# Performance work log

Measured on AMD Instinct MI355X. Metric: run time of the kernel, lower is better.

The kernel has to match this reference:

```python
import jax, jax.numpy as jnp
import numpy as np

N, H, W, SD = 64, 22, 22, 8
HW = H * W


def _conv(x, w, b):
    # 3x3 SAME conv, NCHW / OIHW
    y = jax.lax.conv_general_dilated(x, w, (1, 1), 'SAME',
                                     dimension_numbers=('NCHW', 'OIHW', 'NCHW'))
    return y + b[None, :, None, None]


def _bn(x, g, b, eps=1e-5):
    # BatchNorm2d in training mode: batch statistics over (N, H, W)
    m = jnp.mean(x, axis=(0, 2, 3), keepdims=True)
    v = jnp.var(x, axis=(0, 2, 3), keepdims=True)
    return (x - m) * jax.lax.rsqrt(v + eps) * g[None, :, None, None] + b[None, :, None, None]


def setup_inputs() -> dict:
    key = jax.random.key(0)
    ks = iter(jax.random.split(key, 64))
    def kw(shape):  # kaiming-normal fan_in init
        fan_in = int(np.prod(shape[1:]))
        return jax.random.normal(next(ks), shape, jnp.float32) * np.float32(np.sqrt(2.0 / fan_in))
    d = {
        'cost_volume': jax.random.normal(next(ks), (N, HW, H, W), jnp.float32),
        'state_prev': jax.random.normal(next(ks), (N, SD, H, W), jnp.float32),
        'dimp_score_cur': jax.random.normal(next(ks), (N, 1, H, W), jnp.float32),
    }
    for p in ('cv1', 'cv2'):  # two cost-volume processing stacks: conv(1->8)+BN+ReLU, conv(8->1)+BN
        d[p + '_w1'] = kw((8, 1, 3, 3)); d[p + '_b1'] = jnp.zeros(8, jnp.float32)
        d[p + '_g1'] = jnp.ones(8, jnp.float32); d[p + '_be1'] = jnp.zeros(8, jnp.float32)
        d[p + '_w2'] = kw((1, 8, 3, 3)); d[p + '_b2'] = jnp.zeros(1, jnp.float32)
        d[p + '_g2'] = jnp.ones(1, jnp.float32); d[p + '_be2'] = jnp.zeros(1, jnp.float32)
    d['rp1_w'] = kw((64, SD + 2, 3, 3)); d['rp1_b'] = jnp.zeros(64, jnp.float32)
    d['rp2_w'] = kw((32, 64, 3, 3)); d['rp2_b'] = jnp.zeros(32, jnp.float32)
    d['resp_w'] = kw((1, 32, 3, 3)); d['resp_b'] = jnp.zeros(1, jnp.float32)
    for g_ in ('gru_r', 'gru_u', 'gru_o'):  # ConvGRUCell(input=4, hidden=SD, ksz=3)
        d[g_ + 'w'] = kw((SD, 4 + SD, 3, 3)); d[g_ + 'b'] = jnp.zeros(SD, jnp.float32)
    return d


def _fwd(cost_volume, state_prev, dimp_score_cur,
         cv1_w1, cv1_b1, cv1_g1, cv1_be1, cv1_w2, cv1_b2, cv1_g2, cv1_be2,
         cv2_w1, cv2_b1, cv2_g1, cv2_be1, cv2_w2, cv2_b2, cv2_g2, cv2_be2,
         rp1_w, rp1_b, rp2_w, rp2_b, resp_w, resp_b,
         gru_rw, gru_rb, gru_uw, gru_ub, gru_ow, gru_ob):
    n = cost_volume.shape[0]
    # ---- cost volume processing 1: per-map spatial softmax ----
    x = cost_volume.reshape(-1, 1, H, W)                       # (N*HW, 1, H, W)
    p = jax.nn.relu(_bn(_conv(x, cv1_w1, cv1_b1), cv1_g1, cv1_be1))
    p = _bn(_conv(p, cv1_w2, cv1_b2), cv1_g2, cv1_be2)
    p = jax.nn.softmax(p.reshape(-1, HW), axis=1).reshape(-1, 1, H, W)
    # ---- cost volume processing 2: softmax over source positions ----
    p = jax.nn.relu(_bn(_conv(p, cv2_w1, cv2_b1), cv2_g1, cv2_be1))
    p = _bn(_conv(p, cv2_w2, cv2_b2), cv2_g2, cv2_be2)
    p = jax.nn.softmax(p.reshape(n, HW, H, W), axis=1)         # propagation weights (n, p, h, w)
    # ---- confidence ('max') ----
    conf = jnp.max(p, axis=1, keepdims=True)                   # (N, 1, H, W)
    # ---- state propagation: contract over source positions (no (N,HW,C,H,W) intermediate) ----
    s = state_prev.transpose(0, 2, 3, 1).reshape(n, HW, SD)    # (n, p, d)
    prop_h = jnp.einsum('nphw,npd->ndhw', p, s)                # (N, SD, H, W)
    # ---- response prediction ----
    pin = jnp.concatenate([prop_h, dimp_score_cur, conf], axis=1)   # (N, SD+2, H, W)
    r = jax.nn.relu(_conv(pin, rp1_w, rp1_b))
    r = jax.nn.relu(_conv(r, rp2_w, rp2_b))
    fused = jax.nn.sigmoid(_conv(r, resp_w, resp_b))           # (N, 1, H, W)
    # ---- ConvGRU state update ----
    scores_cat = jnp.concatenate([dimp_score_cur, fused], axis=1)   # (N, 2, H, W)
    pool = jnp.max(scores_cat, axis=(2, 3), keepdims=True)          # adaptive max pool to 1x1
    gin = jnp.concatenate([scores_cat, jnp.broadcast_to(pool, scores_cat.shape)], axis=1)  # (N,4,H,W)
    stacked = jnp.concatenate([gin, prop_h], axis=1)           # (N, 4+SD, H, W)
    upd = jax.nn.sigmoid(_conv(stacked, gru_uw, gru_ub))
    rst = jax.nn.sigmoid(_conv(stacked, gru_rw, gru_rb))
    out = jnp.tanh(_conv(jnp.concatenate([gin, prop_h * rst], axis=1), gru_ow, gru_ob))
    state_new = prop_h * (1.0 - upd) + out * upd               # (N, SD, H, W)
    return jnp.concatenate([fused, state_new], axis=1)         # (N, 1+SD, H, W)


def reference(cost_volume, state_prev, dimp_score_cur,
              cv1_w1, cv1_b1, cv1_g1, cv1_be1, cv1_w2, cv1_b2, cv1_g2, cv1_be2,
              cv2_w1, cv2_b1, cv2_g1, cv2_be1, cv2_w2, cv2_b2, cv2_g2, cv2_be2,
              rp1_w, rp1_b, rp2_w, rp2_b, resp_w, resp_b,
              gru_rw, gru_rb, gru_uw, gru_ub, gru_ow, gru_ob):
    return _fwd(cost_volume, state_prev, dimp_score_cur,
                cv1_w1, cv1_b1, cv1_g1, cv1_be1, cv1_w2, cv1_b2, cv1_g2, cv1_be2,
                cv2_w1, cv2_b1, cv2_g1, cv2_be1, cv2_w2, cv2_b2, cv2_g2, cv2_be2,
                rp1_w, rp1_b, rp2_w, rp2_b, resp_w, resp_b,
                gru_rw, gru_rb, gru_uw, gru_ub, gru_ow, gru_ob)
```

## Files before the change

kernel.cpp:

```cpp
#include <hip/hip_runtime.h>

#define HH 22
#define WW 22
#define HWN 484
#define NBATCH 64
#define SDIM 8
#define NMAPS (NBATCH*HWN)
#define PW 24
#define CELLS 576
#define PADW 24
#define PADSZ (PADW*PADW)
#define INVC (1.f/14992384.f)

#define LD9(A, idx) \
  float x0=(A)[(idx)-PW-1], x1=(A)[(idx)-PW], x2=(A)[(idx)-PW+1], \
        x3=(A)[(idx)-1],    x4=(A)[(idx)],    x5=(A)[(idx)+1], \
        x6=(A)[(idx)+PW-1], x7=(A)[(idx)+PW], x8=(A)[(idx)+PW+1]
#define DOT9W(w9, init) \
  fmaf((w9)[0],x0,fmaf((w9)[1],x1,fmaf((w9)[2],x2,fmaf((w9)[3],x3,fmaf((w9)[4],x4, \
  fmaf((w9)[5],x5,fmaf((w9)[6],x6,fmaf((w9)[7],x7,fmaf((w9)[8],x8,(init))))))))))

#define LOAD_NB(arr, bb) do { \
    nb[0]=(arr)[(bb)-PADW-1]; nb[1]=(arr)[(bb)-PADW]; nb[2]=(arr)[(bb)-PADW+1]; \
    nb[3]=(arr)[(bb)-1];      nb[4]=(arr)[(bb)];      nb[5]=(arr)[(bb)+1]; \
    nb[6]=(arr)[(bb)+PADW-1]; nb[7]=(arr)[(bb)+PADW]; nb[8]=(arr)[(bb)+PADW+1]; } while(0)

__global__ __launch_bounds__(576) void k_stats(const float* __restrict__ src,
    const float* __restrict__ w, const float* __restrict__ b,
    float* __restrict__ Sg, float* __restrict__ Qg)
{
    __shared__ float xin[2][CELLS];
    __shared__ float red[16];
    int tid=threadIdx.x;
    int i=tid/PW, j=tid-i*PW;
    bool inter = (i>=1 && i<=22 && j>=1 && j<=22);
    int p=(i-1)*22+(j-1);
    xin[0][tid]=0.f; xin[1][tid]=0.f;
    float accS[8], accQ[8];
#pragma unroll
    for(int c=0;c<8;++c){ accS[c]=0.f; accQ[c]=0.f; }
    int m0=blockIdx.x*16;
    if(inter) xin[0][tid]=src[(size_t)m0*HWN+p];
    __syncthreads();
    for(int mi=0;mi<16;++mi){
        int cur=mi&1;
        float nx=0.f;
        if(mi<15 && inter) nx=src[(size_t)(m0+mi+1)*HWN+p];
        if(inter){
            LD9(xin[cur], tid);
#pragma unroll
            for(int c=0;c<8;++c){
                float y=DOT9W(w+c*9, b[c]);
                accS[c]+=y; accQ[c]=fmaf(y,y,accQ[c]);
            }
        }
        if(mi<15 && inter) xin[cur^1][tid]=nx;
        __syncthreads();
    }
    if(tid<16) red[tid]=0.f;
    __syncthreads();
#pragma unroll
    for(int c=0;c<8;++c){
        float s=accS[c], q=accQ[c];
        for(int o=32;o;o>>=1){ s+=__shfl_down(s,o); q+=__shfl_down(q,o); }
        if((tid&63)==0){ atomicAdd(&red[c],s); atomicAdd(&red[8+c],q); }
    }
    __syncthreads();
    if(tid<8){ atomicAdd(&Sg[tid],red[tid]); atomicAdd(&Qg[tid],red[8+tid]); }
}

__global__ __launch_bounds__(576) void k_convpair(const float* __restrict__ src, float* __restrict__ Ydst,
    const float* __restrict__ w1, const float* __restrict__ b1,
    const float* __restrict__ Sin, const float* __restrict__ Qin,
    const float* __restrict__ g, const float* __restrict__ be,
    const float* __restrict__ w2, const float* __restrict__ b2,
    float* __restrict__ Sg, float* __restrict__ Qg)
{
    __shared__ float xin[2][CELLS];
    __shared__ float z[8][CELLS];
    __shared__ float scs[8], shs[8];
    __shared__ float red[2];
    int tid=threadIdx.x;
    int i=tid/PW, j=tid-i*PW;
    bool inter = (i>=1 && i<=22 && j>=1 && j<=22);
    int p=(i-1)*22+(j-1);
    xin[0][tid]=0.f; xin[1][tid]=0.f;
#pragma unroll
    for(int c=0;c<8;++c) z[c][tid]=0.f;
    if(tid<8){
        float mean=Sin[tid]*INVC;
        float var=fmaf(-mean,mean,Qin[tid]*INVC);
        float sc=g[tid]*rsqrtf(var+1e-5f);
        scs[tid]=sc; shs[tid]=fmaf(-mean,sc,be[tid]);
    }
    float aS=0.f, aQ=0.f;
    float b2v=b2[0];
    int m0=blockIdx.x*16;
    if(inter) xin[0][tid]=src[(size_t)m0*HWN+p];
    __syncthreads();
    for(int mi=0;mi<16;++mi){
        int cur=mi&1;
        float nx=0.f;
        if(mi<15 && inter) nx=src[(size_t)(m0+mi+1)*HWN+p];
        if(inter){
            LD9(xin[cur], tid);
#pragma unroll
            for(int c=0;c<8;++c){
                float y=DOT9W(w1+c*9, b1[c]);
                y=fmaf(y,scs[c],shs[c]);
                z[c][tid]=y>0.f?y:0.f;
            }
        }
        if(mi<15 && inter) xin[cur^1][tid]=nx;
        __syncthreads();
        if(inter){
            float y=b2v;
#pragma unroll
            for(int c=0;c<8;++c){
                LD9(z[c], tid);
                y=DOT9W(w2+c*9, y);
            }
            Ydst[(size_t)(m0+mi)*HWN+p]=y;
            aS+=y; aQ=fmaf(y,y,aQ);
        }
        __syncthreads();
    }
    if(tid<2) red[tid]=0.f;
    __syncthreads();
    for(int o=32;o;o>>=1){ aS+=__shfl_down(aS,o); aQ+=__shfl_down(aQ,o); }
    if((tid&63)==0){ atomicAdd(&red[0],aS); atomicAdd(&red[1],aQ); }
    __syncthreads();
    if(tid==0){ atomicAdd(Sg,red[0]); atomicAdd(Qg,red[1]); }
}

__global__ __launch_bounds__(576) void k_smax_stats(float* __restrict__ Y,
    const float* __restrict__ S2, const float* __restrict__ Q2,
    const float* __restrict__ g2, const float* __restrict__ be2,
    const float* __restrict__ w, const float* __restrict__ b,
    float* __restrict__ Sg, float* __restrict__ Qg)
{
    __shared__ float xin[CELLS];
    __shared__ float red9[9];
    __shared__ float red[16];
    int tid=threadIdx.x;
    int i=tid/PW, j=tid-i*PW;
    bool inter = (i>=1 && i<=22 && j>=1 && j<=22);
    int p=(i-1)*22+(j-1);
    float mean=S2[0]*INVC;
    float var=fmaf(-mean,mean,Q2[0]*INVC);
    float a=g2[0]*rsqrtf(var+1e-5f);
    float sh=fmaf(-mean,a,be2[0]);
    xin[tid]=0.f;
    float accS[8], accQ[8];
#pragma unroll
    for(int c=0;c<8;++c){ accS[c]=0.f; accQ[c]=0.f; }
    int m0=blockIdx.x*16;
    for(int mi=0;mi<16;++mi){
        size_t off=(size_t)(m0+mi)*HWN+p;
        float e = inter ? __expf(fmaf(Y[off],a,sh)) : 0.f;
        float part=e;
        for(int o=32;o;o>>=1) part+=__shfl_down(part,o);
        if((tid&63)==0) red9[tid>>6]=part;
        xin[tid]=e;
        __syncthreads();
        float sum=red9[0]+red9[1]+red9[2]+red9[3]+red9[4]+red9[5]+red9[6]+red9[7]+red9[8];
        float inv=1.f/sum;
        if(inter){
            Y[off]=e*inv;
            LD9(xin, tid);
#pragma unroll
            for(int c=0;c<8;++c){
                float d=DOT9W(w+c*9, 0.f);
                float y=fmaf(inv,d,b[c]);
                accS[c]+=y; accQ[c]=fmaf(y,y,accQ[c]);
            }
        }
        __syncthreads();
    }
    if(tid<16) red[tid]=0.f;
    __syncthreads();
#pragma unroll
    for(int c=0;c<8;++c){
        float s=accS[c], q=accQ[c];
        for(int o=32;o;o>>=1){ s+=__shfl_down(s,o); q+=__shfl_down(q,o); }
        if((tid&63)==0){ atomicAdd(&red[c],s); atomicAdd(&red[8+c],q); }
    }
    __syncthreads();
    if(tid<8){ atomicAdd(&Sg[tid],red[tid]); atomicAdd(&Qg[tid],red[8+tid]); }
}

__global__ __launch_bounds__(512) void k_prop(const float* __restrict__ Y,
    const float* __restrict__ S4, const float* __restrict__ Q4,
    const float* __restrict__ g4, const float* __restrict__ be4,
    const float* __restrict__ state, float* __restrict__ prop, float* __restrict__ conf)
{
    int n=blockIdx.x;
    __shared__ float sst[8*HWN];
    __shared__ float part[4][121][10];
    int tid=threadIdx.x;
    for(int q=tid;q<8*HWN;q+=512) sst[q]=state[(size_t)n*8*HWN + q];
    __syncthreads();
    int tq=tid&127, pc=tid>>7;
    int t=blockIdx.y*121+tq;
    float mean=S4[0]*INVC;
    float var=fmaf(-mean,mean,Q4[0]*INVC);
    float a=g4[0]*rsqrtf(var+1e-5f);
    float sh=fmaf(-mean,a,be4[0]);
    if(tq<121){
        const float* col = Y + (size_t)n*HWN*HWN + t + (size_t)pc*121*HWN;
        const float* sp = sst + pc*121;
        float mx=-1e30f, ssum=0.f;
        float acc[8];
#pragma unroll
        for(int d=0;d<8;++d) acc[d]=0.f;
#pragma unroll 4
        for(int p=0;p<121;++p){
            float v=fmaf(col[(size_t)p*HWN], a, sh);
            float e=__expf(v);
            mx=fmaxf(mx,v); ssum+=e;
#pragma unroll
            for(int d=0;d<8;++d) acc[d]=fmaf(e, sp[d*HWN+p], acc[d]);
        }
        part[pc][tq][0]=ssum; part[pc][tq][1]=mx;
#pragma unroll
        for(int d=0;d<8;++d) part[pc][tq][2+d]=acc[d];
    }
    __syncthreads();
    if(pc==0 && tq<121){
        float ssum=part[0][tq][0]+part[1][tq][0]+part[2][tq][0]+part[3][tq][0];
        float mx=fmaxf(fmaxf(part[0][tq][1],part[1][tq][1]),fmaxf(part[2][tq][1],part[3][tq][1]));
        float inv=1.f/ssum;
        conf[(size_t)n*HWN+t]=__expf(mx)*inv;
#pragma unroll
        for(int d=0;d<8;++d){
            float acd=part[0][tq][2+d]+part[1][tq][2+d]+part[2][tq][2+d]+part[3][tq][2+d];
            prop[((size_t)n*8+d)*HWN+t]=acd*inv;
        }
    }
}

__global__ __launch_bounds__(256) void k_rp1(const float* __restrict__ prop,
    const float* __restrict__ dimp, const float* __restrict__ conf,
    const float* __restrict__ wf, const float* __restrict__ bfv, float* __restrict__ R1)
{
    int n=blockIdx.x, g=blockIdx.y;
    __shared__ float pin[10*PADSZ];
    int tid=threadIdx.x;
    for(int i=tid;i<10*PADSZ;i+=256) pin[i]=0.f;
    __syncthreads();
    for(int p=tid;p<HWN;p+=256){
        int i=p/WW, j=p-i*WW; int aa=(i+1)*PADW+j+1;
#pragma unroll
        for(int d=0;d<8;++d) pin[d*PADSZ+aa]=prop[((size_t)n*8+d)*HWN+p];
        pin[8*PADSZ+aa]=dimp[(size_t)n*HWN+p];
        pin[9*PADSZ+aa]=conf[(size_t)n*HWN+p];
    }
    __syncthreads();
    const float* wg = wf + (size_t)(g*16)*90;
    for(int p=tid;p<HWN;p+=256){
        int i=p/WW, j=p-i*WW; int aa=(i+1)*PADW+j+1;
        float acc[16];
#pragma unroll
        for(int o=0;o<16;++o) acc[o]=bfv[g*16+o];
#pragma unroll
        for(int c=0;c<10;++c){
            float nb[9]; int bb=c*PADSZ+aa;
            LOAD_NB(pin, bb);
#pragma unroll
            for(int o=0;o<16;++o){
                const float* w=wg+o*90+c*9;
#pragma unroll
                for(int t=0;t<9;++t) acc[o]=fmaf(w[t], nb[t], acc[o]);
            }
        }
#pragma unroll
        for(int o=0;o<16;++o){
            float y=acc[o];
            R1[((size_t)n*64 + g*16+o)*HWN+p]= y>0.f?y:0.f;
        }
    }
}

__global__ __launch_bounds__(512) void k_rp2(const float* __restrict__ R1,
    const float* __restrict__ wf, const float* __restrict__ bfv, float* __restrict__ R2)
{
    int n=blockIdx.x, g=blockIdx.y;
    __shared__ float xc[16*PADSZ];
    int tid=threadIdx.x;
    for(int i=tid;i<16*PADSZ;i+=512) xc[i]=0.f;
    int p=tid; bool act = p<HWN;
    int i=p/WW, j=p-i*WW, aa=(i+1)*PADW+j+1;
    float acc[8];
#pragma unroll
    for(int o=0;o<8;++o) acc[o]=0.f;
    for(int k=0;k<4;++k){
        __syncthreads();
        for(int q=tid;q<16*HWN;q+=512){
            int ic=q/HWN, pp=q-ic*HWN;
            int ii=pp/WW, jj=pp-ii*WW;
            xc[ic*PADSZ+(ii+1)*PADW+jj+1]=R1[((size_t)n*64 + k*16+ic)*HWN+pp];
        }
        __syncthreads();
        if(act){
#pragma unroll
            for(int ic=0;ic<16;++ic){
                float nb[9]; int bb=ic*PADSZ+aa;
                LOAD_NB(xc, bb);
#pragma unroll
                for(int o=0;o<8;++o){
                    const float* w = wf + ((size_t)(g*8+o)*64 + k*16+ic)*9;
#pragma unroll
                    for(int t=0;t<9;++t) acc[o]=fmaf(w[t], nb[t], acc[o]);
                }
            }
        }
    }
    if(act){
#pragma unroll
        for(int o=0;o<8;++o){
            float y=acc[o]+bfv[g*8+o];
            R2[((size_t)n*32+g*8+o)*HWN+p]= y>0.f?y:0.f;
        }
    }
}

__global__ __launch_bounds__(512) void k_resp(const float* __restrict__ R2,
    const float* __restrict__ wf, const float* __restrict__ bfv,
    const float* __restrict__ dimp, float* __restrict__ fused,
    float* __restrict__ pool, float* __restrict__ out)
{
    int n=blockIdx.x;
    __shared__ float xc[16*PADSZ];
    __shared__ float redf[8], redd[8];
    int tid=threadIdx.x;
    for(int i=tid;i<16*PADSZ;i+=512) xc[i]=0.f;
    int p=tid; bool act=p<HWN;
    int i=p/WW, j=p-i*WW, aa=(i+1)*PADW+j+1;
    float acc=0.f;
    for(int k=0;k<2;++k){
        __syncthreads();
        for(int q=tid;q<16*HWN;q+=512){
            int ic=q/HWN, pp=q-ic*HWN;
            int ii=pp/WW, jj=pp-ii*WW;
            xc[ic*PADSZ+(ii+1)*PADW+jj+1]=R2[((size_t)n*32+k*16+ic)*HWN+pp];
        }
        __syncthreads();
        if(act){
#pragma unroll
            for(int ic=0;ic<16;++ic){
                float nb[9]; int bb=ic*PADSZ+aa;
                LOAD_NB(xc, bb);
                const float* w=wf+(size_t)(k*16+ic)*9;
#pragma unroll
                for(int t=0;t<9;++t) acc=fmaf(w[t], nb[t], acc);
            }
        }
    }
    float fval=-1e30f, dval=-1e30f;
    if(act){
        float y=acc+bfv[0];
        float s=1.f/(1.f+__expf(-y));
        fused[(size_t)n*HWN+p]=s;
        out[(size_t)n*9*HWN+p]=s;
        fval=s;
        dval=dimp[(size_t)n*HWN+p];
    }
    int lane=tid&63, wid=tid>>6;
    for(int o=32;o;o>>=1){ fval=fmaxf(fval,__shfl_xor(fval,o)); dval=fmaxf(dval,__shfl_xor(dval,o)); }
    if(lane==0){ redf[wid]=fval; redd[wid]=dval; }
    __syncthreads();
    if(tid==0){
        float fm=redf[0], dm=redd[0];
        for(int q=1;q<8;++q){ fm=fmaxf(fm,redf[q]); dm=fmaxf(dm,redd[q]); }
        pool[n*2+0]=dm; pool[n*2+1]=fm;
    }
}

__global__ __launch_bounds__(512) void k_gru(const float* __restrict__ dimp,
    const float* __restrict__ fused, const float* __restrict__ pool,
    const float* __restrict__ prop,
    const float* __restrict__ wr, const float* __restrict__ br,
    const float* __restrict__ wu, const float* __restrict__ bu,
    const float* __restrict__ wo, const float* __restrict__ bo,
    float* __restrict__ out)
{
    int n=blockIdx.x;
    __shared__ float sg[12*PADSZ];
    __shared__ float pr[8*PADSZ];
    int tid=threadIdx.x;
    for(int i=tid;i<12*PADSZ;i+=512) sg[i]=0.f;
    for(int i=tid;i<8*PADSZ;i+=512) pr[i]=0.f;
    __syncthreads();
    float p0=pool[n*2+0], p1=pool[n*2+1];
    for(int p=tid;p<HWN;p+=512){
        int i=p/WW, j=p-i*WW, aa=(i+1)*PADW+j+1;
        sg[0*PADSZ+aa]=dimp[(size_t)n*HWN+p];
        sg[1*PADSZ+aa]=fused[(size_t)n*HWN+p];
        sg[2*PADSZ+aa]=p0;
        sg[3*PADSZ+aa]=p1;
#pragma unroll
        for(int d=0;d<8;++d) sg[(4+d)*PADSZ+aa]=prop[((size_t)n*8+d)*HWN+p];
    }
    __syncthreads();
    int p=tid; bool act=p<HWN;
    int i=p/WW, j=p-i*WW, aa=(i+1)*PADW+j+1;
    float upd[8];
    if(act){
        float ua[8], ra[8];
#pragma unroll
        for(int o=0;o<8;++o){ ua[o]=bu[o]; ra[o]=br[o]; }
#pragma unroll
        for(int ic=0;ic<12;++ic){
            float nb[9]; int bb=ic*PADSZ+aa;
            LOAD_NB(sg, bb);
#pragma unroll
            for(int o=0;o<8;++o){
                const float* wup=wu+((size_t)o*12+ic)*9;
                const float* wrp=wr+((size_t)o*12+ic)*9;
#pragma unroll
                for(int t=0;t<9;++t){
                    ua[o]=fmaf(wup[t], nb[t], ua[o]);
                    ra[o]=fmaf(wrp[t], nb[t], ra[o]);
                }
            }
        }
#pragma unroll
        for(int o=0;o<8;++o){
            upd[o]=1.f/(1.f+__expf(-ua[o]));
            float rst=1.f/(1.f+__expf(-ra[o]));
            pr[o*PADSZ+aa]=sg[(4+o)*PADSZ+aa]*rst;
        }
    }
    __syncthreads();
    if(act){
        float oa[8];
#pragma unroll
        for(int o=0;o<8;++o) oa[o]=bo[o];
#pragma unroll
        for(int ic=0;ic<12;++ic){
            const float* srcp = (ic<4)? (sg+ic*PADSZ) : (pr+(ic-4)*PADSZ);
            float nb[9]; int bb=aa;
            LOAD_NB(srcp, bb);
#pragma unroll
            for(int o=0;o<8;++o){
                const float* wop=wo+((size_t)o*12+ic)*9;
#pragma unroll
                for(int t=0;t<9;++t) oa[o]=fmaf(wop[t], nb[t], oa[o]);
            }
        }
#pragma unroll
        for(int o=0;o<8;++o){
            float od=tanhf(oa[o]);
            float ph=sg[(4+o)*PADSZ+aa];
            float sn=ph*(1.f-upd[o])+od*upd[o];
            out[((size_t)n*9+1+o)*HWN+p]=sn;
        }
    }
}

extern "C" void kernel_launch(void* const* d_in, const int* in_sizes, int n_in,
                              void* d_out, int out_size, void* d_ws, size_t ws_size,
                              hipStream_t stream)
{
    (void)in_sizes; (void)n_in; (void)out_size; (void)ws_size;
    float* ws=(float*)d_ws;
    float* Y     = ws;
    float* PROP  = ws + 14992384;
    float* CONF  = PROP + 247808;
    float* FUSED = CONF + 30976;
    float* POOL  = FUSED + 30976;
    float* STATS = POOL + 128;
    float* R1    = ws;
    float* R2    = ws + 4000000;

    const float* cv    = (const float*)d_in[0];
    const float* state = (const float*)d_in[1];
    const float* dimp  = (const float*)d_in[2];
    float* out = (float*)d_out;

    hipMemsetAsync(STATS, 0, 36*sizeof(float), stream);

    float *S1=STATS,*Q1=STATS+8,*S2=STATS+16,*Q2=STATS+17,*S3=STATS+18,*Q3=STATS+26,*S4=STATS+34,*Q4=STATS+35;

    const float* cv1_w1=(const float*)d_in[3];  const float* cv1_b1=(const float*)d_in[4];
    const float* cv1_g1=(const float*)d_in[5];  const float* cv1_be1=(const float*)d_in[6];
    const float* cv1_w2=(const float*)d_in[7];  const float* cv1_b2=(const float*)d_in[8];
    const float* cv1_g2=(const float*)d_in[9];  const float* cv1_be2=(const float*)d_in[10];
    const float* cv2_w1=(const float*)d_in[11]; const float* cv2_b1=(const float*)d_in[12];
    const float* cv2_g1=(const float*)d_in[13]; const float* cv2_be1=(const float*)d_in[14];
    const float* cv2_w2=(const float*)d_in[15]; const float* cv2_b2=(const float*)d_in[16];
    const float* cv2_g2=(const float*)d_in[17]; const float* cv2_be2=(const float*)d_in[18];
    const float* rp1_w=(const float*)d_in[19];  const float* rp1_b=(const float*)d_in[20];
    const float* rp2_w=(const float*)d_in[21];  const float* rp2_b=(const float*)d_in[22];
    const float* resp_w=(const float*)d_in[23]; const float* resp_b=(const float*)d_in[24];
    const float* gru_rw=(const float*)d_in[25]; const float* gru_rb=(const float*)d_in[26];
    const float* gru_uw=(const float*)d_in[27]; const float* gru_ub=(const float*)d_in[28];
    const float* gru_ow=(const float*)d_in[29]; const float* gru_ob=(const float*)d_in[30];

    k_stats<<<1936,576,0,stream>>>(cv, cv1_w1, cv1_b1, S1, Q1);
    k_convpair<<<1936,576,0,stream>>>(cv, Y, cv1_w1, cv1_b1, S1, Q1, cv1_g1, cv1_be1,
                                      cv1_w2, cv1_b2, S2, Q2);
    k_smax_stats<<<1936,576,0,stream>>>(Y, S2, Q2, cv1_g2, cv1_be2, cv2_w1, cv2_b1, S3, Q3);
    k_convpair<<<1936,576,0,stream>>>(Y, Y, cv2_w1, cv2_b1, S3, Q3, cv2_g1, cv2_be1,
                                      cv2_w2, cv2_b2, S4, Q4);
    k_prop<<<dim3(64,4),512,0,stream>>>(Y, S4, Q4, cv2_g2, cv2_be2, state, PROP, CONF);
    k_rp1<<<dim3(64,4),256,0,stream>>>(PROP, dimp, CONF, rp1_w, rp1_b, R1);
    k_rp2<<<dim3(64,4),512,0,stream>>>(R1, rp2_w, rp2_b, R2);
    k_resp<<<64,512,0,stream>>>(R2, resp_w, resp_b, dimp, FUSED, POOL, out);
    k_gru<<<64,512,0,stream>>>(dimp, FUSED, POOL, PROP,
                               gru_rw, gru_rb, gru_uw, gru_ub, gru_ow, gru_ob, out);
}
```

Before: 969.7 us.

## Process each cost-volume map per wavefront with 2x2 register tiles

The four cost-volume kernels change from one 576-thread block per 16 maps, synchronizing with __syncthreads for every map, to 256-thread blocks in which each wavefront owns its own maps and its own padded shared buffer. Each lane loads maps with float4 reads and computes a 2x2 output tile from a 4x4 register window, so neighbouring taps are reused across outputs. The shared layout adds a row skew to reduce bank conflicts, and the softmax sum becomes a single wavefront xor-shuffle reduction. In exchange the intermediate z buffer is written and read inside the same wavefront without any barrier, relying on lockstep execution within the wavefront, and the indexing is considerably more complex.

```diff
diff --git a/kernel.cpp b/kernel.cpp
--- a/kernel.cpp
+++ b/kernel.cpp
@@ -6,187 +6,278 @@
 #define NBATCH 64
 #define SDIM 8
 #define NMAPS (NBATCH*HWN)
-#define PW 24
-#define CELLS 576
 #define PADW 24
-#define PADSZ (PADW*PADW)
+#define PADSZ 576
 #define INVC (1.f/14992384.f)
 
-#define LD9(A, idx) \
-  float x0=(A)[(idx)-PW-1], x1=(A)[(idx)-PW], x2=(A)[(idx)-PW+1], \
-        x3=(A)[(idx)-1],    x4=(A)[(idx)],    x5=(A)[(idx)+1], \
-        x6=(A)[(idx)+PW-1], x7=(A)[(idx)+PW], x8=(A)[(idx)+PW+1]
-#define DOT9W(w9, init) \
-  fmaf((w9)[0],x0,fmaf((w9)[1],x1,fmaf((w9)[2],x2,fmaf((w9)[3],x3,fmaf((w9)[4],x4, \
-  fmaf((w9)[5],x5,fmaf((w9)[6],x6,fmaf((w9)[7],x7,fmaf((w9)[8],x8,(init))))))))))
+#define CPW 25
+#define XSZ 600
+
+__device__ __forceinline__ int cellof(int r,int c){
+    int rr=r+1, cc=c+1;
+    return rr*CPW + cc + ((rr>>1)&1);
+}
+
+struct Geo {
+    int stc[8];
+    int tbA[4], tbB[4];
+    int zA0,zA1,zB0,zB1;
+    int rA0,rB0;
+    bool hasB;
+};
+
+__device__ __forceinline__ void mkgeo(int lane, Geo& G){
+    G.hasB = (lane < 57);
+#pragma unroll
+    for(int k=0;k<4;++k){ int p=lane*4+k; int r=p/22; G.stc[k]=cellof(r,p-r*22); }
+#pragma unroll
+    for(int k=0;k<4;++k){
+        int p=(lane+64)*4+k; int r=p/22;
+        G.stc[4+k]= G.hasB ? cellof(r,p-r*22) : 0;
+    }
+    int prA=lane/11, pcA=lane-prA*11;
+    int pB = G.hasB ? lane+64 : 0;
+    int prB=pB/11, pcB=pB-prB*11;
+#pragma unroll
+    for(int kr=0;kr<4;++kr){
+        G.tbA[kr]=cellof(2*prA-1+kr, 2*pcA-1);
+        G.tbB[kr]=cellof(2*prB-1+kr, 2*pcB-1);
+    }
+    G.zA0=cellof(2*prA,2*pcA);   G.zA1=cellof(2*prA+1,2*pcA);
+    G.zB0=cellof(2*prB,2*pcB);   G.zB1=cellof(2*prB+1,2*pcB);
+    G.rA0=2*prA*22+2*pcA;        G.rB0=2*prB*22+2*pcB;
+}
+
+__device__ __forceinline__ void ldtaps(const float* xs, const int tb[4], float T[4][4]){
+#pragma unroll
+    for(int kr=0;kr<4;++kr)
+#pragma unroll
+        for(int kc=0;kc<4;++kc) T[kr][kc]=xs[tb[kr]+kc];
+}
+
+__device__ __forceinline__ void conv1p(const float T[4][4], const float* __restrict__ w9, float init,
+                                       float&y00,float&y01,float&y10,float&y11){
+    y00=init;y01=init;y10=init;y11=init;
+#pragma unroll
+    for(int kr=0;kr<3;++kr)
+#pragma unroll
+        for(int kc=0;kc<3;++kc){
+            float wv=w9[kr*3+kc];
+            y00=fmaf(wv,T[kr][kc],y00);     y01=fmaf(wv,T[kr][kc+1],y01);
+            y10=fmaf(wv,T[kr+1][kc],y10);   y11=fmaf(wv,T[kr+1][kc+1],y11);
+        }
+}
+__device__ __forceinline__ void conv2p(const float T[4][4], const float* __restrict__ w9,
+                                       float&y00,float&y01,float&y10,float&y11){
+#pragma unroll
+    for(int kr=0;kr<3;++kr)
+#pragma unroll
+        for(int kc=0;kc<3;++kc){
+            float wv=w9[kr*3+kc];
+            y00=fmaf(wv,T[kr][kc],y00);     y01=fmaf(wv,T[kr][kc+1],y01);
+            y10=fmaf(wv,T[kr+1][kc],y10);   y11=fmaf(wv,T[kr+1][kc+1],y11);
+        }
+}
 
 #define LOAD_NB(arr, bb) do { \
     nb[0]=(arr)[(bb)-PADW-1]; nb[1]=(arr)[(bb)-PADW]; nb[2]=(arr)[(bb)-PADW+1]; \
     nb[3]=(arr)[(bb)-1];      nb[4]=(arr)[(bb)];      nb[5]=(arr)[(bb)+1]; \
     nb[6]=(arr)[(bb)+PADW-1]; nb[7]=(arr)[(bb)+PADW]; nb[8]=(arr)[(bb)+PADW+1]; } while(0)
 
-__global__ __launch_bounds__(576) void k_stats(const float* __restrict__ src,
+__global__ __launch_bounds__(256) void k_stats(const float* __restrict__ src,
     const float* __restrict__ w, const float* __restrict__ b,
     float* __restrict__ Sg, float* __restrict__ Qg)
 {
-    __shared__ float xin[2][CELLS];
-    __shared__ float red[16];
-    int tid=threadIdx.x;
-    int i=tid/PW, j=tid-i*PW;
-    bool inter = (i>=1 && i<=22 && j>=1 && j<=22);
-    int p=(i-1)*22+(j-1);
-    xin[0][tid]=0.f; xin[1][tid]=0.f;
+    __shared__ float xsall[4*XSZ];
+    __shared__ float redS[8], redQ[8];
+    int tid=threadIdx.x, lane=tid&63, wv=tid>>6;
+    float* xs=xsall+wv*XSZ;
+    for(int q=tid;q<4*XSZ;q+=256) xsall[q]=0.f;
+    if(tid<8){ redS[tid]=0.f; redQ[tid]=0.f; }
+    __syncthreads();
+    Geo G; mkgeo(lane,G);
     float accS[8], accQ[8];
 #pragma unroll
     for(int c=0;c<8;++c){ accS[c]=0.f; accQ[c]=0.f; }
-    int m0=blockIdx.x*16;
-    if(inter) xin[0][tid]=src[(size_t)m0*HWN+p];
-    __syncthreads();
-    for(int mi=0;mi<16;++mi){
-        int cur=mi&1;
-        float nx=0.f;
-        if(mi<15 && inter) nx=src[(size_t)(m0+mi+1)*HWN+p];
-        if(inter){
-            LD9(xin[cur], tid);
-#pragma unroll
-            for(int c=0;c<8;++c){
-                float y=DOT9W(w+c*9, b[c]);
-                accS[c]+=y; accQ[c]=fmaf(y,y,accQ[c]);
-            }
-        }
-        if(mi<15 && inter) xin[cur^1][tid]=nx;
-        __syncthreads();
-    }
-    if(tid<16) red[tid]=0.f;
-    __syncthreads();
+    int W=blockIdx.x*4+wv;
+    for(int mi=0;mi<4;++mi){
+        const float4* s4=(const float4*)(src+(size_t)(W*4+mi)*HWN);
+        float4 va=s4[lane];
+        float4 vb= G.hasB ? s4[lane+64] : make_float4(0.f,0.f,0.f,0.f);
+        xs[G.stc[0]]=va.x; xs[G.stc[1]]=va.y; xs[G.stc[2]]=va.z; xs[G.stc[3]]=va.w;
+        if(G.hasB){ xs[G.stc[4]]=vb.x; xs[G.stc[5]]=vb.y; xs[G.stc[6]]=vb.z; xs[G.stc[7]]=vb.w; }
+        float tA[4][4], tB[4][4];
+        ldtaps(xs,G.tbA,tA); ldtaps(xs,G.tbB,tB);
+#pragma unroll
+        for(int c=0;c<8;++c){
+            const float* w9=w+c*9; float bc=b[c];
+            float a00,a01,a10,a11,q00,q01,q10,q11;
+            conv1p(tA,w9,bc,a00,a01,a10,a11);
+            conv1p(tB,w9,bc,q00,q01,q10,q11);
+            float s=a00+a01+a10+a11;
+            float q=fmaf(a00,a00,fmaf(a01,a01,fmaf(a10,a10,a11*a11)));
+            if(G.hasB){
+                s+=q00+q01+q10+q11;
+                q+=fmaf(q00,q00,fmaf(q01,q01,fmaf(q10,q10,q11*q11)));
+            }
+            accS[c]+=s; accQ[c]+=q;
+        }
+    }
 #pragma unroll
     for(int c=0;c<8;++c){
         float s=accS[c], q=accQ[c];
         for(int o=32;o;o>>=1){ s+=__shfl_down(s,o); q+=__shfl_down(q,o); }
-        if((tid&63)==0){ atomicAdd(&red[c],s); atomicAdd(&red[8+c],q); }
-    }
-    __syncthreads();
-    if(tid<8){ atomicAdd(&Sg[tid],red[tid]); atomicAdd(&Qg[tid],red[8+tid]); }
-}
-
-__global__ __launch_bounds__(576) void k_convpair(const float* __restrict__ src, float* __restrict__ Ydst,
+        if(lane==0){ atomicAdd(&redS[c],s); atomicAdd(&redQ[c],q); }
+    }
+    __syncthreads();
+    if(tid<8){ atomicAdd(&Sg[tid],redS[tid]); atomicAdd(&Qg[tid],redQ[tid]); }
+}
+
+__global__ __launch_bounds__(256) void k_convpair(const float* __restrict__ src, float* __restrict__ Ydst,
     const float* __restrict__ w1, const float* __restrict__ b1,
     const float* __restrict__ Sin, const float* __restrict__ Qin,
     const float* __restrict__ g, const float* __restrict__ be,
     const float* __restrict__ w2, const float* __restrict__ b2,
     float* __restrict__ Sg, float* __restrict__ Qg)
 {
-    __shared__ float xin[2][CELLS];
-    __shared__ float z[8][CELLS];
-    __shared__ float scs[8], shs[8];
-    __shared__ float red[2];
-    int tid=threadIdx.x;
-    int i=tid/PW, j=tid-i*PW;
-    bool inter = (i>=1 && i<=22 && j>=1 && j<=22);
-    int p=(i-1)*22+(j-1);
-    xin[0][tid]=0.f; xin[1][tid]=0.f;
-#pragma unroll
-    for(int c=0;c<8;++c) z[c][tid]=0.f;
-    if(tid<8){
-        float mean=Sin[tid]*INVC;
-        float var=fmaf(-mean,mean,Qin[tid]*INVC);
-        float sc=g[tid]*rsqrtf(var+1e-5f);
-        scs[tid]=sc; shs[tid]=fmaf(-mean,sc,be[tid]);
-    }
+    __shared__ float xsall[4*XSZ];
+    __shared__ float zsall[4*XSZ];
+    __shared__ float redS[2];
+    int tid=threadIdx.x, lane=tid&63, wv=tid>>6;
+    float* xs=xsall+wv*XSZ;
+    float* zs=zsall+wv*XSZ;
+    for(int q=tid;q<4*XSZ;q+=256){ xsall[q]=0.f; zsall[q]=0.f; }
+    if(tid<2) redS[tid]=0.f;
+    __syncthreads();
+    Geo G; mkgeo(lane,G);
+    float scv[8], shv[8];
+#pragma unroll
+    for(int c=0;c<8;++c){
+        float mean=Sin[c]*INVC;
+        float var=fmaf(-mean,mean,Qin[c]*INVC);
+        float sc=g[c]*rsqrtf(var+1e-5f);
+        scv[c]=sc; shv[c]=fmaf(-mean,sc,be[c]);
+    }
+    float b2v=b2[0];
     float aS=0.f, aQ=0.f;
-    float b2v=b2[0];
-    int m0=blockIdx.x*16;
-    if(inter) xin[0][tid]=src[(size_t)m0*HWN+p];
-    __syncthreads();
-    for(int mi=0;mi<16;++mi){
-        int cur=mi&1;
-        float nx=0.f;
-        if(mi<15 && inter) nx=src[(size_t)(m0+mi+1)*HWN+p];
-        if(inter){
-            LD9(xin[cur], tid);
-#pragma unroll
-            for(int c=0;c<8;++c){
-                float y=DOT9W(w1+c*9, b1[c]);
-                y=fmaf(y,scs[c],shs[c]);
-                z[c][tid]=y>0.f?y:0.f;
-            }
-        }
-        if(mi<15 && inter) xin[cur^1][tid]=nx;
-        __syncthreads();
-        if(inter){
-            float y=b2v;
-#pragma unroll
-            for(int c=0;c<8;++c){
-                LD9(z[c], tid);
-                y=DOT9W(w2+c*9, y);
-            }
-            Ydst[(size_t)(m0+mi)*HWN+p]=y;
-            aS+=y; aQ=fmaf(y,y,aQ);
-        }
-        __syncthreads();
-    }
-    if(tid<2) red[tid]=0.f;
-    __syncthreads();
+    int W=blockIdx.x*4+wv;
+    for(int mi=0;mi<4;++mi){
+        size_t mbase=(size_t)(W*4+mi)*HWN;
+        const float4* s4=(const float4*)(src+mbase);
+        float4 va=s4[lane];
+        float4 vb= G.hasB ? s4[lane+64] : make_float4(0.f,0.f,0.f,0.f);
+        xs[G.stc[0]]=va.x; xs[G.stc[1]]=va.y; xs[G.stc[2]]=va.z; xs[G.stc[3]]=va.w;
+        if(G.hasB){ xs[G.stc[4]]=vb.x; xs[G.stc[5]]=vb.y; xs[G.stc[6]]=vb.z; xs[G.stc[7]]=vb.w; }
+        float tA[4][4], tB[4][4];
+        ldtaps(xs,G.tbA,tA); ldtaps(xs,G.tbB,tB);
+        float oA00=b2v,oA01=b2v,oA10=b2v,oA11=b2v;
+        float oB00=b2v,oB01=b2v,oB10=b2v,oB11=b2v;
+#pragma unroll
+        for(int c=0;c<8;++c){
+            const float* w9=w1+c*9; float bc=b1[c];
+            float a00,a01,a10,a11,q00,q01,q10,q11;
+            conv1p(tA,w9,bc,a00,a01,a10,a11);
+            conv1p(tB,w9,bc,q00,q01,q10,q11);
+            float sc=scv[c], sh=shv[c];
+            a00=fmaf(a00,sc,sh); a01=fmaf(a01,sc,sh); a10=fmaf(a10,sc,sh); a11=fmaf(a11,sc,sh);
+            a00=a00>0.f?a00:0.f; a01=a01>0.f?a01:0.f; a10=a10>0.f?a10:0.f; a11=a11>0.f?a11:0.f;
+            zs[G.zA0]=a00; zs[G.zA0+1]=a01; zs[G.zA1]=a10; zs[G.zA1+1]=a11;
+            if(G.hasB){
+                q00=fmaf(q00,sc,sh); q01=fmaf(q01,sc,sh); q10=fmaf(q10,sc,sh); q11=fmaf(q11,sc,sh);
+                q00=q00>0.f?q00:0.f; q01=q01>0.f?q01:0.f; q10=q10>0.f?q10:0.f; q11=q11>0.f?q11:0.f;
+                zs[G.zB0]=q00; zs[G.zB0+1]=q01; zs[G.zB1]=q10; zs[G.zB1+1]=q11;
+            }
+            float zA[4][4], zB[4][4];
+            ldtaps(zs,G.tbA,zA); ldtaps(zs,G.tbB,zB);
+            const float* v9=w2+c*9;
+            conv2p(zA,v9,oA00,oA01,oA10,oA11);
+            conv2p(zB,v9,oB00,oB01,oB10,oB11);
+        }
+        float* yp=Ydst+mbase;
+        yp[G.rA0]=oA00; yp[G.rA0+1]=oA01; yp[G.rA0+22]=oA10; yp[G.rA0+23]=oA11;
+        aS+=oA00+oA01+oA10+oA11;
+        aQ=fmaf(oA00,oA00,fmaf(oA01,oA01,fmaf(oA10,oA10,fmaf(oA11,oA11,aQ))));
+        if(G.hasB){
+            yp[G.rB0]=oB00; yp[G.rB0+1]=oB01; yp[G.rB0+22]=oB10; yp[G.rB0+23]=oB11;
+            aS+=oB00+oB01+oB10+oB11;
+            aQ=fmaf(oB00,oB00,fmaf(oB01,oB01,fmaf(oB10,oB10,fmaf(oB11,oB11,aQ))));
+        }
+    }
     for(int o=32;o;o>>=1){ aS+=__shfl_down(aS,o); aQ+=__shfl_down(aQ,o); }
-    if((tid&63)==0){ atomicAdd(&red[0],aS); atomicAdd(&red[1],aQ); }
-    __syncthreads();
-    if(tid==0){ atomicAdd(Sg,red[0]); atomicAdd(Qg,red[1]); }
-}
-
-__global__ __launch_bounds__(576) void k_smax_stats(float* __restrict__ Y,
+    if(lane==0){ atomicAdd(&redS[0],aS); atomicAdd(&redS[1],aQ); }
+    __syncthreads();
+    if(tid==0) atomicAdd(Sg,redS[0]);
+    if(tid==1) atomicAdd(Qg,redS[1]);
+}
+
+__global__ __launch_bounds__(256) void k_smax_stats(float* __restrict__ Y,
     const float* __restrict__ S2, const float* __restrict__ Q2,
     const float* __restrict__ g2, const float* __restrict__ be2,
     const float* __restrict__ w, const float* __restrict__ b,
     float* __restrict__ Sg, float* __restrict__ Qg)
 {
-    __shared__ float xin[CELLS];
-    __shared__ float red9[9];
-    __shared__ float red[16];
-    int tid=threadIdx.x;
-    int i=tid/PW, j=tid-i*PW;
-    bool inter = (i>=1 && i<=22 && j>=1 && j<=22);
-    int p=(i-1)*22+(j-1);
+    __shared__ float xsall[4*XSZ];
+    __shared__ float redS[8], redQ[8];
+    int tid=threadIdx.x, lane=tid&63, wv=tid>>6;
+    float* xs=xsall+wv*XSZ;
+    for(int q=tid;q<4*XSZ;q+=256) xsall[q]=0.f;
+    if(tid<8){ redS[tid]=0.f; redQ[tid]=0.f; }
+    __syncthreads();
+    Geo G; mkgeo(lane,G);
     float mean=S2[0]*INVC;
     float var=fmaf(-mean,mean,Q2[0]*INVC);
     float a=g2[0]*rsqrtf(var+1e-5f);
     float sh=fmaf(-mean,a,be2[0]);
-    xin[tid]=0.f;
     float accS[8], accQ[8];
 #pragma unroll
     for(int c=0;c<8;++c){ accS[c]=0.f; accQ[c]=0.f; }
-    int m0=blockIdx.x*16;
-    for(int mi=0;mi<16;++mi){
-        size_t off=(size_t)(m0+mi)*HWN+p;
-        float e = inter ? __expf(fmaf(Y[off],a,sh)) : 0.f;
-        float part=e;
-        for(int o=32;o;o>>=1) part+=__shfl_down(part,o);
-        if((tid&63)==0) red9[tid>>6]=part;
-        xin[tid]=e;
-        __syncthreads();
-        float sum=red9[0]+red9[1]+red9[2]+red9[3]+red9[4]+red9[5]+red9[6]+red9[7]+red9[8];
-        float inv=1.f/sum;
-        if(inter){
-            Y[off]=e*inv;
-            LD9(xin, tid);
-#pragma unroll
-            for(int c=0;c<8;++c){
-                float d=DOT9W(w+c*9, 0.f);
-                float y=fmaf(inv,d,b[c]);
-                accS[c]+=y; accQ[c]=fmaf(y,y,accQ[c]);
-            }
-        }
-        __syncthreads();
-    }
-    if(tid<16) red[tid]=0.f;
-    __syncthreads();
+    int W=blockIdx.x*4+wv;
+    for(int mi=0;mi<4;++mi){
+        size_t mbase=(size_t)(W*4+mi)*HWN;
+        float4* y4=(float4*)(Y+mbase);
+        float4 va=y4[lane];
+        float e0=__expf(fmaf(va.x,a,sh)), e1=__expf(fmaf(va.y,a,sh));
+        float e2=__expf(fmaf(va.z,a,sh)), e3=__expf(fmaf(va.w,a,sh));
+        float e4=0.f,e5=0.f,e6=0.f,e7=0.f;
+        if(G.hasB){
+            float4 vb=y4[lane+64];
+            e4=__expf(fmaf(vb.x,a,sh)); e5=__expf(fmaf(vb.y,a,sh));
+            e6=__expf(fmaf(vb.z,a,sh)); e7=__expf(fmaf(vb.w,a,sh));
+        }
+        xs[G.stc[0]]=e0; xs[G.stc[1]]=e1; xs[G.stc[2]]=e2; xs[G.stc[3]]=e3;
+        if(G.hasB){ xs[G.stc[4]]=e4; xs[G.stc[5]]=e5; xs[G.stc[6]]=e6; xs[G.stc[7]]=e7; }
+        float ms=(e0+e1)+(e2+e3)+((e4+e5)+(e6+e7));
+        for(int o=32;o;o>>=1) ms+=__shfl_xor(ms,o);
+        float inv=1.f/ms;
+        y4[lane]=make_float4(e0*inv,e1*inv,e2*inv,e3*inv);
+        if(G.hasB) y4[lane+64]=make_float4(e4*inv,e5*inv,e6*inv,e7*inv);
+        float tA[4][4], tB[4][4];
+        ldtaps(xs,G.tbA,tA); ldtaps(xs,G.tbB,tB);
+#pragma unroll
+        for(int c=0;c<8;++c){
+            const float* w9=w+c*9; float bc=b[c];
+            float a00,a01,a10,a11,q00,q01,q10,q11;
+            conv1p(tA,w9,0.f,a00,a01,a10,a11);
+            conv1p(tB,w9,0.f,q00,q01,q10,q11);
+            a00=fmaf(inv,a00,bc); a01=fmaf(inv,a01,bc); a10=fmaf(inv,a10,bc); a11=fmaf(inv,a11,bc);
+            float s=a00+a01+a10+a11;
+            float q=fmaf(a00,a00,fmaf(a01,a01,fmaf(a10,a10,a11*a11)));
+            if(G.hasB){
+                q00=fmaf(inv,q00,bc); q01=fmaf(inv,q01,bc); q10=fmaf(inv,q10,bc); q11=fmaf(inv,q11,bc);
+                s+=q00+q01+q10+q11;
+                q+=fmaf(q00,q00,fmaf(q01,q01,fmaf(q10,q10,q11*q11)));
+            }
+            accS[c]+=s; accQ[c]+=q;
+        }
+    }
 #pragma unroll
     for(int c=0;c<8;++c){
         float s=accS[c], q=accQ[c];
         for(int o=32;o;o>>=1){ s+=__shfl_down(s,o); q+=__shfl_down(q,o); }
-        if((tid&63)==0){ atomicAdd(&red[c],s); atomicAdd(&red[8+c],q); }
-    }
-    __syncthreads();
-    if(tid<8){ atomicAdd(&Sg[tid],red[tid]); atomicAdd(&Qg[tid],red[8+tid]); }
+        if(lane==0){ atomicAdd(&redS[c],s); atomicAdd(&redQ[c],q); }
+    }
+    __syncthreads();
+    if(tid<8){ atomicAdd(&Sg[tid],redS[tid]); atomicAdd(&Qg[tid],redQ[tid]); }
 }
 
 __global__ __launch_bounds__(512) void k_prop(const float* __restrict__ Y,
@@ -497,11 +588,11 @@
     const float* gru_uw=(const float*)d_in[27]; const float* gru_ub=(const float*)d_in[28];
     const float* gru_ow=(const float*)d_in[29]; const float* gru_ob=(const float*)d_in[30];
 
-    k_stats<<<1936,576,0,stream>>>(cv, cv1_w1, cv1_b1, S1, Q1);
-    k_convpair<<<1936,576,0,stream>>>(cv, Y, cv1_w1, cv1_b1, S1, Q1, cv1_g1, cv1_be1,
+    k_stats<<<1936,256,0,stream>>>(cv, cv1_w1, cv1_b1, S1, Q1);
+    k_convpair<<<1936,256,0,stream>>>(cv, Y, cv1_w1, cv1_b1, S1, Q1, cv1_g1, cv1_be1,
                                       cv1_w2, cv1_b2, S2, Q2);
-    k_smax_stats<<<1936,576,0,stream>>>(Y, S2, Q2, cv1_g2, cv1_be2, cv2_w1, cv2_b1, S3, Q3);
-    k_convpair<<<1936,576,0,stream>>>(Y, Y, cv2_w1, cv2_b1, S3, Q3, cv2_g1, cv2_be1,
+    k_smax_stats<<<1936,256,0,stream>>>(Y, S2, Q2, cv1_g2, cv1_be2, cv2_w1, cv2_b1, S3, Q3);
+    k_convpair<<<1936,256,0,stream>>>(Y, Y, cv2_w1, cv2_b1, S3, Q3, cv2_g1, cv2_be1,
                                       cv2_w2, cv2_b2, S4, Q4);
     k_prop<<<dim3(64,4),512,0,stream>>>(Y, S4, Q4, cv2_g2, cv2_be2, state, PROP, CONF);
     k_rp1<<<dim3(64,4),256,0,stream>>>(PROP, dimp, CONF, rp1_w, rp1_b, R1);
```

New measurement: 902.6 us. 6.9% less time.
